# Performance work log

Hardware: AMD Instinct MI355X
Metric: run time of the kernel (lower is better)

## Reference

```python
import jax, jax.numpy as jnp
import numpy as np

N, K, D, GH = 19683, 26, 64, 32  # cells (27^3), max neighbors, state_size, gating hidden


def setup_inputs() -> dict:
    key = jax.random.key(0)
    ks = jax.random.split(key, 10)
    s = 0.1
    return {
        "current_state": jax.random.normal(ks[0], (N, D), jnp.float32),
        "neighbor_states": jax.random.normal(ks[1], (N, K, D), jnp.float32),
        "neighbor_cat": jax.random.randint(ks[2], (N, K), 0, 3),  # 0=local,1=functional,2=distant
        "W_local": s * jax.random.normal(ks[3], (2 * D, D), jnp.float32),
        "b_local": jnp.zeros((D,), jnp.float32),
        "W_f1": s * jax.random.normal(ks[4], (2 * D, 2 * D), jnp.float32),
        "b_f1": jnp.zeros((2 * D,), jnp.float32),
        "W_f2": s * jax.random.normal(ks[5], (2 * D, D), jnp.float32),
        "b_f2": jnp.zeros((D,), jnp.float32),
        "W_c1": s * jax.random.normal(ks[6], (2 * D, 2 * D), jnp.float32),
        "b_c1": jnp.zeros((2 * D,), jnp.float32),
        "W_c2": s * jax.random.normal(ks[7], (2 * D, D), jnp.float32),
        "b_c2": jnp.zeros((D,), jnp.float32),
        "W_g1": s * jax.random.normal(ks[8], (2 * D, GH), jnp.float32),
        "b_g1": jnp.zeros((GH,), jnp.float32),
        "W_g2": s * jax.random.normal(ks[9], (GH, 3), jnp.float32),
        "b_g2": jnp.zeros((3,), jnp.float32),
    }


def _masked_mean(nb, mask):
    # nb: [N,K,D], mask: [N,K] float -> mean over selected neighbors, count
    cnt = mask.sum(axis=1, keepdims=True)  # [N,1]
    mean = (nb * mask[..., None]).sum(axis=1) / jnp.maximum(cnt, 1.0)
    return mean, cnt


def reference(current_state, neighbor_states, neighbor_cat, W_local, b_local,
              W_f1, b_f1, W_f2, b_f2, W_c1, b_c1, W_c2, b_c2,
              W_g1, b_g1, W_g2, b_g2):
    cur, nb, cat = current_state, neighbor_states, neighbor_cat
    m_loc = (cat == 0).astype(cur.dtype)
    m_fun = (cat == 1).astype(cur.dtype)
    m_dst = (cat == 2).astype(cur.dtype)
    mean_l, cnt_l = _masked_mean(nb, m_loc)
    mean_f, cnt_f = _masked_mean(nb, m_fun)
    mean_d, cnt_d = _masked_mean(nb, m_dst)

    # local expert: SimpleLinear on [cur, local neighbor aggregate]
    out_l = jnp.tanh(jnp.concatenate([cur, mean_l], -1) @ W_local + b_local)
    out_l = jnp.where(cnt_l > 0, out_l, 0.0)  # zeros when no local neighbors

    # functional expert: HybridGNN-style 2-layer message MLP
    h = jnp.tanh(jnp.concatenate([cur, mean_f], -1) @ W_f1 + b_f1)
    out_f = jnp.tanh(h @ W_f2 + b_f2)
    out_f = jnp.where(cnt_f > 0, out_f, 0.0)

    # distant expert: lightweight CNF, 3 Euler integration steps
    x = cur
    dt = 1.0 / 3.0
    for _ in range(3):  # fixed integration_steps, not a data-dim loop
        v = jnp.tanh(jnp.concatenate([x, mean_d], -1) @ W_c1 + b_c1)
        x = x + dt * jnp.tanh(v @ W_c2 + b_c2)
    out_d = jnp.where(cnt_d > 0, x, 0.0)

    # gating network over [cur, neighbor_activity]
    act = nb.mean(axis=1)  # [N,D]
    g = jnp.tanh(jnp.concatenate([cur, act], -1) @ W_g1 + b_g1) @ W_g2 + b_g2
    w = jax.nn.softmax(g, axis=-1)  # [N,3]

    combined = w[:, 0:1] * out_l + w[:, 1:2] * out_f + w[:, 2:3] * out_d
    return combined, w
```

## Files before the change

kernel.cpp:

```cpp
#include <hip/hip_runtime.h>


#define NCELL 19683
#define KNB 26
#define NGROUP 1231
#define AGG_BLOCKS 2461
#define RP_BLOCKS 30
#define CUR_BLOCKS 616

typedef short bf16x8 __attribute__((ext_vector_type(8)));
typedef float f32x4 __attribute__((ext_vector_type(4)));

#define MEANB (NCELL * 64 * 2)
#define OFF_ML 0
#define OFF_MF (1 * MEANB)
#define OFF_MD (2 * MEANB)
#define OFF_ACT (3 * MEANB)
#define OFF_FLAGS (4 * MEANB)
#define OFF_RP (OFF_FLAGS + NCELL * 16)
#define OFF_CUR (OFF_RP + 120 * 1024)

#define FB_L 0
#define FB_F1 16
#define FB_F2 48
#define FB_C1 64
#define FB_C2 96
#define FB_G1 112

__device__ __forceinline__ unsigned short f2b(float f) {
  unsigned u; __builtin_memcpy(&u, &f, 4);
  u += 0x7FFFu + ((u >> 16) & 1u);
  return (unsigned short)(u >> 16);
}

__global__ __launch_bounds__(256) void k_prep(
    const float* __restrict__ nbp, const int* __restrict__ catp,
    const float* __restrict__ Wl, const float* __restrict__ Wf1,
    const float* __restrict__ Wf2, const float* __restrict__ Wc1,
    const float* __restrict__ Wc2, const float* __restrict__ Wg1,
    const float* __restrict__ curp, char* __restrict__ ws) {
  int bid = blockIdx.x;
  int tid = threadIdx.x;
  int lane = tid & 63;
  int wid = tid >> 6;

  if (bid < AGG_BLOCKS) {
    int half = lane >> 5;
    int l31 = lane & 31;
    int cell = bid * 8 + wid * 2 + half;
    int cc = min(cell, NCELL - 1);
    int myc = (l31 < KNB) ? catp[cc * KNB + l31] : -1;
    unsigned long long bl0 = __ballot(myc == 0);
    unsigned long long bl1 = __ballot(myc == 1);
    unsigned long long bl2 = __ballot(myc == 2);
    unsigned m0 = (unsigned)(bl0 >> (half * 32));
    unsigned m1 = (unsigned)(bl1 >> (half * 32));
    unsigned m2 = (unsigned)(bl2 >> (half * 32));
    float cl = (float)__popc(m0), cf = (float)__popc(m1), cd = (float)__popc(m2);

    const float* nbf = nbp + (size_t)cc * (KNB * 64) + l31 * 2;
    float sl0 = 0, sl1 = 0, sf0 = 0, sf1 = 0, sd0 = 0, sd1 = 0, sa0 = 0, sa1 = 0;
#pragma unroll
    for (int k = 0; k < KNB; k++) {
      float2 vf = *(const float2*)(nbf + k * 64);
      float v0 = vf.x, v1 = vf.y;
      int c = __shfl(myc, half * 32 + k);
      sa0 += v0; sa1 += v1;
      sl0 += (c == 0) ? v0 : 0.0f; sl1 += (c == 0) ? v1 : 0.0f;
      sf0 += (c == 1) ? v0 : 0.0f; sf1 += (c == 1) ? v1 : 0.0f;
      sd0 += (c == 2) ? v0 : 0.0f; sd1 += (c == 2) ? v1 : 0.0f;
    }
    float rl = 1.0f / fmaxf(cl, 1.0f);
    float rf = 1.0f / fmaxf(cf, 1.0f);
    float rd = 1.0f / fmaxf(cd, 1.0f);
    const float r26 = 1.0f / 26.0f;
    if (cell < NCELL) {
      int off = cell * 128 + l31 * 4;
      *(unsigned*)(ws + OFF_ML + off) = (unsigned)f2b(sl0 * rl) | ((unsigned)f2b(sl1 * rl) << 16);
      *(unsigned*)(ws + OFF_MF + off) = (unsigned)f2b(sf0 * rf) | ((unsigned)f2b(sf1 * rf) << 16);
      *(unsigned*)(ws + OFF_MD + off) = (unsigned)f2b(sd0 * rd) | ((unsigned)f2b(sd1 * rd) << 16);
      *(unsigned*)(ws + OFF_ACT + off) = (unsigned)f2b(sa0 * r26) | ((unsigned)f2b(sa1 * r26) << 16);
      if (l31 == 0) {
        float4 fl;
        fl.x = (cl > 0.0f) ? 1.0f : 0.0f;
        fl.y = (cf > 0.0f) ? 1.0f : 0.0f;
        fl.z = (cd > 0.0f) ? 1.0f : 0.0f;
        fl.w = 0.0f;
        *(float4*)(ws + OFF_FLAGS + cell * 16) = fl;
      }
    }
  } else if (bid < AGG_BLOCKS + RP_BLOCKS) {
    int frag = (bid - AGG_BLOCKS) * 4 + wid;
    if (frag >= 120) return;
    const float* src; int Nd, lf;
    if (frag < 16)       { src = Wl;  Nd = 64;  lf = frag; }
    else if (frag < 48)  { src = Wf1; Nd = 128; lf = frag - 16; }
    else if (frag < 64)  { src = Wf2; Nd = 64;  lf = frag - 48; }
    else if (frag < 96)  { src = Wc1; Nd = 128; lf = frag - 64; }
    else if (frag < 112) { src = Wc2; Nd = 64;  lf = frag - 96; }
    else                 { src = Wg1; Nd = 32;  lf = frag - 112; }
    int nt = lf >> 2, kt = lf & 3;
    int n = nt * 16 + (lane & 15);
    int k0 = kt * 32 + (lane >> 4) * 8;
    unsigned short o[8] __attribute__((aligned(16)));
#pragma unroll
    for (int j = 0; j < 8; j++) o[j] = f2b(src[(k0 + j) * Nd + n]);
    *(uint4*)(ws + OFF_RP + ((size_t)frag * 64 + lane) * 16) = *(const uint4*)o;
  } else {
    int idx = (bid - AGG_BLOCKS - RP_BLOCKS) * 256 + tid;
    if (idx >= NCELL * 8) return;
    float4 a = ((const float4*)curp)[idx * 2];
    float4 b = ((const float4*)curp)[idx * 2 + 1];
    uint4 o;
    o.x = (unsigned)f2b(a.x) | ((unsigned)f2b(a.y) << 16);
    o.y = (unsigned)f2b(a.z) | ((unsigned)f2b(a.w) << 16);
    o.z = (unsigned)f2b(b.x) | ((unsigned)f2b(b.y) << 16);
    o.w = (unsigned)f2b(b.z) | ((unsigned)f2b(b.w) << 16);
    ((uint4*)(ws + OFF_CUR))[idx] = o;
  }
}

__device__ __forceinline__ void stage64(const uint4* __restrict__ src, int g, uint4* dst, int lane) {
#pragma unroll
  for (int i = 0; i < 2; i++) {
    int idx = min(g * 128 + i * 64 + lane, NCELL * 8 - 1);
    uint4 v = src[idx];
    int local = i * 64 + lane;
    int cell = local >> 3, c = local & 7;
    dst[cell * 8 + (c ^ (cell & 7))] = v;
  }
}
__device__ __forceinline__ void afrags2(const uint4* lo, const uint4* hi, int m, int q, bf16x8* a) {
#pragma unroll
  for (int kt = 0; kt < 4; kt++) {
    const uint4* b = (kt < 2) ? lo : hi;
    int ch = ((kt & 1) * 4 + q) ^ (m & 7);
    a[kt] = *(const bf16x8*)&b[m * 8 + ch];
  }
}
__device__ __forceinline__ void afragsS(const uint4* sb, int m, int q, bf16x8* a) {
#pragma unroll
  for (int kt = 0; kt < 4; kt++) {
    int ch = (kt * 4 + q) ^ m;
    a[kt] = *(const bf16x8*)&sb[m * 16 + ch];
  }
}
template <int NT>
__device__ __forceinline__ void gemmN(const bf16x8* __restrict__ wf, int fb, const bf16x8* a,
                                      int lane, f32x4* out) {
#pragma unroll
  for (int nt = 0; nt < NT; nt++) {
    f32x4 acc = {0.f, 0.f, 0.f, 0.f};
#pragma unroll
    for (int kt = 0; kt < 4; kt++) {
      bf16x8 b = wf[(fb + nt * 4 + kt) * 64 + lane];
      acc = __builtin_amdgcn_mfma_f32_16x16x32_bf16(a[kt], b, acc, 0, 0, 0);
    }
    out[nt] = acc;
  }
}
__device__ __forceinline__ void store_sb(uint4* sb, int cell, int feat, float v) {
  ((unsigned short*)&sb[cell * 16 + ((feat >> 3) ^ cell)])[feat & 7] = f2b(v);
}
__device__ __forceinline__ void store_xb(uint4* xb, int cell, int feat, float v) {
  ((unsigned short*)&xb[cell * 8 + ((feat >> 3) ^ (cell & 7))])[feat & 7] = f2b(v);
}

__global__ __launch_bounds__(256) void k_mlp(
    const float* __restrict__ curp,
    const float* __restrict__ bl_, const float* __restrict__ bf1_,
    const float* __restrict__ bf2_, const float* __restrict__ bc1_,
    const float* __restrict__ bc2_, const float* __restrict__ bg1_,
    const float* __restrict__ Wg2, const float* __restrict__ bg2_,
    const char* __restrict__ ws, float* __restrict__ outp) {
  __shared__ uint4 smem[4 * 640];
  int tid = threadIdx.x, lane = tid & 63, wv = tid >> 6;
  int g = blockIdx.x * 4 + wv;
  if (g >= NGROUP) return;
  uint4* wbase = smem + wv * 640;
  uint4* curb = wbase;
  uint4* mb = wbase + 128;
  uint4* xb = wbase + 256;
  uint4* sb = wbase + 384;

  const unsigned short* curh = (const unsigned short*)(ws + OFF_CUR);
  int m = lane & 15, q = lane >> 4;
  const bf16x8* wf = (const bf16x8*)(ws + OFF_RP);
  bf16x8 a[4];

  stage64((const uint4*)curh, g, curb, lane);
  stage64((const uint4*)(ws + OFF_ML), g, mb, lane);
  afrags2(curb, mb, m, q, a);
  f32x4 ol[4];
  gemmN<4>(wf, FB_L, a, lane, ol);
#pragma unroll
  for (int nt = 0; nt < 4; nt++) {
    float bb = bl_[nt * 16 + m];
#pragma unroll
    for (int r = 0; r < 4; r++) ol[nt][r] = tanhf(ol[nt][r] + bb);
  }

  stage64((const uint4*)(ws + OFF_MF), g, mb, lane);
  afrags2(curb, mb, m, q, a);
  f32x4 h8[8];
  gemmN<8>(wf, FB_F1, a, lane, h8);
#pragma unroll
  for (int nt = 0; nt < 8; nt++) {
    float bb = bf1_[nt * 16 + m];
#pragma unroll
    for (int r = 0; r < 4; r++) store_sb(sb, q * 4 + r, nt * 16 + m, tanhf(h8[nt][r] + bb));
  }
  afragsS(sb, m, q, a);
  f32x4 of[4];
  gemmN<4>(wf, FB_F2, a, lane, of);
#pragma unroll
  for (int nt = 0; nt < 4; nt++) {
    float bb = bf2_[nt * 16 + m];
#pragma unroll
    for (int r = 0; r < 4; r++) of[nt][r] = tanhf(of[nt][r] + bb);
  }

  stage64((const uint4*)(ws + OFF_ACT), g, mb, lane);
  afrags2(curb, mb, m, q, a);
  f32x4 gh[2];
  gemmN<2>(wf, FB_G1, a, lane, gh);
#pragma unroll
  for (int nt = 0; nt < 2; nt++) {
    float bb = bg1_[nt * 16 + m];
#pragma unroll
    for (int r = 0; r < 4; r++) gh[nt][r] = tanhf(gh[nt][r] + bb);
  }
  float w2v[2][3];
#pragma unroll
  for (int nt = 0; nt < 2; nt++)
#pragma unroll
    for (int t = 0; t < 3; t++) w2v[nt][t] = Wg2[(nt * 16 + m) * 3 + t];
  float bg2v[3];
#pragma unroll
  for (int t = 0; t < 3; t++) bg2v[t] = bg2_[t];
  float w0[4], w1[4], w2[4];
#pragma unroll
  for (int r = 0; r < 4; r++) {
    float gv[3];
#pragma unroll
    for (int t = 0; t < 3; t++) {
      float p = gh[0][r] * w2v[0][t] + gh[1][r] * w2v[1][t];
      p += __shfl_xor(p, 1); p += __shfl_xor(p, 2); p += __shfl_xor(p, 4); p += __shfl_xor(p, 8);
      gv[t] = p + bg2v[t];
    }
    float mx = fmaxf(gv[0], fmaxf(gv[1], gv[2]));
    float e0 = expf(gv[0] - mx), e1 = expf(gv[1] - mx), e2 = expf(gv[2] - mx);
    float rs = 1.0f / (e0 + e1 + e2);
    w0[r] = e0 * rs; w1[r] = e1 * rs; w2[r] = e2 * rs;
    int cell = g * 16 + q * 4 + r;
    if (cell < NCELL && m < 3) {
      float wsel = (m == 0) ? w0[r] : (m == 1) ? w1[r] : w2[r];
      outp[(size_t)NCELL * 64 + cell * 3 + m] = wsel;
    }
  }

  stage64((const uint4*)(ws + OFF_MD), g, mb, lane);
  float xr[4][4];
#pragma unroll
  for (int nt = 0; nt < 4; nt++)
#pragma unroll
    for (int r = 0; r < 4; r++) {
      int cell = min(g * 16 + q * 4 + r, NCELL - 1);
      xr[nt][r] = curp[(size_t)cell * 64 + nt * 16 + m];
    }
  for (int step = 0; step < 3; step++) {
#pragma unroll
    for (int nt = 0; nt < 4; nt++)
#pragma unroll
      for (int r = 0; r < 4; r++) store_xb(xb, q * 4 + r, nt * 16 + m, xr[nt][r]);
    afrags2(xb, mb, m, q, a);
    f32x4 v8[8];
    gemmN<8>(wf, FB_C1, a, lane, v8);
#pragma unroll
    for (int nt = 0; nt < 8; nt++) {
      float bb = bc1_[nt * 16 + m];
#pragma unroll
      for (int r = 0; r < 4; r++) store_sb(sb, q * 4 + r, nt * 16 + m, tanhf(v8[nt][r] + bb));
    }
    afragsS(sb, m, q, a);
    f32x4 dx[4];
    gemmN<4>(wf, FB_C2, a, lane, dx);
#pragma unroll
    for (int nt = 0; nt < 4; nt++) {
      float bb = bc2_[nt * 16 + m];
#pragma unroll
      for (int r = 0; r < 4; r++) xr[nt][r] += (1.0f / 3.0f) * tanhf(dx[nt][r] + bb);
    }
  }

  float4 flg[4];
  const float4* flp = (const float4*)(ws + OFF_FLAGS);
#pragma unroll
  for (int r = 0; r < 4; r++) flg[r] = flp[min(g * 16 + q * 4 + r, NCELL - 1)];
#pragma unroll
  for (int nt = 0; nt < 4; nt++)
#pragma unroll
    for (int r = 0; r < 4; r++) {
      float res = w0[r] * flg[r].x * ol[nt][r] + w1[r] * flg[r].y * of[nt][r] +
                  w2[r] * flg[r].z * xr[nt][r];
      int cell = g * 16 + q * 4 + r;
      if (cell < NCELL) outp[(size_t)cell * 64 + nt * 16 + m] = res;
    }
}

extern "C" void kernel_launch(void* const* d_in, const int* in_sizes, int n_in,
                              void* d_out, int out_size, void* d_ws, size_t ws_size,
                              hipStream_t stream) {
  const float* cur = (const float*)d_in[0];
  const float* nb  = (const float*)d_in[1];
  const int* cat   = (const int*)d_in[2];
  const float* Wl  = (const float*)d_in[3];
  const float* bl  = (const float*)d_in[4];
  const float* Wf1 = (const float*)d_in[5];
  const float* bf1 = (const float*)d_in[6];
  const float* Wf2 = (const float*)d_in[7];
  const float* bf2 = (const float*)d_in[8];
  const float* Wc1 = (const float*)d_in[9];
  const float* bc1 = (const float*)d_in[10];
  const float* Wc2 = (const float*)d_in[11];
  const float* bc2 = (const float*)d_in[12];
  const float* Wg1 = (const float*)d_in[13];
  const float* bg1 = (const float*)d_in[14];
  const float* Wg2 = (const float*)d_in[15];
  const float* bg2 = (const float*)d_in[16];
  char* ws = (char*)d_ws;
  float* outp = (float*)d_out;

  k_prep<<<AGG_BLOCKS + RP_BLOCKS + CUR_BLOCKS, 256, 0, stream>>>(
      nb, cat, Wl, Wf1, Wf2, Wc1, Wc2, Wg1, cur, ws);
  k_mlp<<<(NGROUP + 3) / 4, 256, 0, stream>>>(cur, bl, bf1, bf2, bc1, bc2, bg1, Wg2, bg2,
                                              (const char*)ws, outp);
}
```

Baseline: 303.1 us.

## Fuse neighbor aggregation into MLP kernel and split experts across waves

Neighbor aggregation now runs inside the main kernel, and the means go straight into shared memory, so the bf16 mean buffers no longer make a round trip through global memory. Each 256-thread block handles 16 cells, with work split by wave: wave 0 runs the local expert and gating, wave 1 the functional expert, and waves 2-3 share the CNF steps, synchronising through barriers. tanhf/expf are replaced by fast exp/rcp approximations. The cost is extra block barriers, idle waves 0-1 during the CNF steps, and slightly lower accuracy in tanh.

```diff
diff --git a/kernel.cpp b/kernel.cpp
--- a/kernel.cpp
+++ b/kernel.cpp
@@ -3,22 +3,10 @@
 
 #define NCELL 19683
 #define KNB 26
-#define NGROUP 1231
-#define AGG_BLOCKS 2461
-#define RP_BLOCKS 30
-#define CUR_BLOCKS 616
+#define NGRP 1231
 
 typedef short bf16x8 __attribute__((ext_vector_type(8)));
 typedef float f32x4 __attribute__((ext_vector_type(4)));
-
-#define MEANB (NCELL * 64 * 2)
-#define OFF_ML 0
-#define OFF_MF (1 * MEANB)
-#define OFF_MD (2 * MEANB)
-#define OFF_ACT (3 * MEANB)
-#define OFF_FLAGS (4 * MEANB)
-#define OFF_RP (OFF_FLAGS + NCELL * 16)
-#define OFF_CUR (OFF_RP + 120 * 1024)
 
 #define FB_L 0
 #define FB_F1 16
@@ -32,280 +20,299 @@
   u += 0x7FFFu + ((u >> 16) & 1u);
   return (unsigned short)(u >> 16);
 }
-
-__global__ __launch_bounds__(256) void k_prep(
-    const float* __restrict__ nbp, const int* __restrict__ catp,
+__device__ __forceinline__ unsigned pack2(float x, float y) {
+  return (unsigned)f2b(x) | ((unsigned)f2b(y) << 16);
+}
+__device__ __forceinline__ float tanh_fast(float x) {
+  float e = __expf(2.0f * x);
+  return 1.0f - 2.0f * __builtin_amdgcn_rcpf(e + 1.0f);
+}
+
+__global__ __launch_bounds__(256) void k_repack(
     const float* __restrict__ Wl, const float* __restrict__ Wf1,
     const float* __restrict__ Wf2, const float* __restrict__ Wc1,
     const float* __restrict__ Wc2, const float* __restrict__ Wg1,
-    const float* __restrict__ curp, char* __restrict__ ws) {
-  int bid = blockIdx.x;
-  int tid = threadIdx.x;
-  int lane = tid & 63;
-  int wid = tid >> 6;
-
-  if (bid < AGG_BLOCKS) {
-    int half = lane >> 5;
-    int l31 = lane & 31;
-    int cell = bid * 8 + wid * 2 + half;
-    int cc = min(cell, NCELL - 1);
-    int myc = (l31 < KNB) ? catp[cc * KNB + l31] : -1;
-    unsigned long long bl0 = __ballot(myc == 0);
-    unsigned long long bl1 = __ballot(myc == 1);
-    unsigned long long bl2 = __ballot(myc == 2);
-    unsigned m0 = (unsigned)(bl0 >> (half * 32));
-    unsigned m1 = (unsigned)(bl1 >> (half * 32));
-    unsigned m2 = (unsigned)(bl2 >> (half * 32));
+    char* __restrict__ ws) {
+  int frag = blockIdx.x * 4 + (threadIdx.x >> 6);
+  int lane = threadIdx.x & 63;
+  if (frag >= 120) return;
+  const float* src; int Nd, lf;
+  if (frag < 16)       { src = Wl;  Nd = 64;  lf = frag; }
+  else if (frag < 48)  { src = Wf1; Nd = 128; lf = frag - 16; }
+  else if (frag < 64)  { src = Wf2; Nd = 64;  lf = frag - 48; }
+  else if (frag < 96)  { src = Wc1; Nd = 128; lf = frag - 64; }
+  else if (frag < 112) { src = Wc2; Nd = 64;  lf = frag - 96; }
+  else                 { src = Wg1; Nd = 32;  lf = frag - 112; }
+  int nt = lf >> 2, kt = lf & 3;
+  int n = nt * 16 + (lane & 15);
+  int k0 = kt * 32 + (lane >> 4) * 8;
+  unsigned short o[8] __attribute__((aligned(16)));
+#pragma unroll
+  for (int j = 0; j < 8; j++) o[j] = f2b(src[(k0 + j) * Nd + n]);
+  *(uint4*)(ws + ((size_t)frag * 64 + lane) * 16) = *(const uint4*)o;
+}
+
+__device__ __forceinline__ void afrags2(const uint4* lo, const uint4* hi, int m, int q, bf16x8* a) {
+#pragma unroll
+  for (int kt = 0; kt < 4; kt++) {
+    const uint4* b = (kt < 2) ? lo : hi;
+    int ch = ((kt & 1) * 4 + q) ^ (m & 7);
+    a[kt] = *(const bf16x8*)&b[m * 8 + ch];
+  }
+}
+__device__ __forceinline__ void afragsS(const uint4* sb, int m, int q, bf16x8* a) {
+#pragma unroll
+  for (int kt = 0; kt < 4; kt++) {
+    int ch = (kt * 4 + q) ^ m;
+    a[kt] = *(const bf16x8*)&sb[m * 16 + ch];
+  }
+}
+template <int NT>
+__device__ __forceinline__ void gemmN(const bf16x8* __restrict__ wf, int fb, const bf16x8* a,
+                                      int lane, f32x4* out) {
+#pragma unroll
+  for (int nt = 0; nt < NT; nt++) {
+    f32x4 acc = {0.f, 0.f, 0.f, 0.f};
+#pragma unroll
+    for (int kt = 0; kt < 4; kt++) {
+      bf16x8 b = wf[(fb + nt * 4 + kt) * 64 + lane];
+      acc = __builtin_amdgcn_mfma_f32_16x16x32_bf16(a[kt], b, acc, 0, 0, 0);
+    }
+    out[nt] = acc;
+  }
+}
+__device__ __forceinline__ void store_sb(uint4* sb, int cell, int feat, float v) {
+  ((unsigned short*)&sb[cell * 16 + ((feat >> 3) ^ cell)])[feat & 7] = f2b(v);
+}
+__device__ __forceinline__ void store_xb(uint4* xb, int cell, int feat, float v) {
+  ((unsigned short*)&xb[cell * 8 + ((feat >> 3) ^ (cell & 7))])[feat & 7] = f2b(v);
+}
+
+__global__ __launch_bounds__(256, 4) void k_main(
+    const float* __restrict__ curp, const float* __restrict__ nbp, const int* __restrict__ catp,
+    const float* __restrict__ bl_, const float* __restrict__ bf1_, const float* __restrict__ bf2_,
+    const float* __restrict__ bc1_, const float* __restrict__ bc2_, const float* __restrict__ bg1_,
+    const float* __restrict__ Wg2, const float* __restrict__ bg2_,
+    const char* __restrict__ ws, float* __restrict__ outp) {
+  __shared__ uint4 smem[2080];
+  uint4* curb = smem;
+  uint4* mlb  = smem + 128;
+  uint4* mfb  = smem + 256;
+  uint4* mdb  = smem + 384;
+  uint4* actb = smem + 512;
+  uint4* xb   = smem + 640;
+  uint4* sbF  = smem + 768;
+  uint4* sbC  = smem + 1024;
+  float* outL = (float*)(smem + 1280);
+  float* outF = (float*)(smem + 1536);
+  float* outD = (float*)(smem + 1792);
+  float4* flagsb = (float4*)(smem + 2048);
+  float4* wvalsb = (float4*)(smem + 2064);
+
+  int tid = threadIdx.x, lane = tid & 63, wv = tid >> 6;
+  int g = blockIdx.x;
+
+  {
+    int cq = lane >> 4, fq = lane & 15;
+    int cellLoc = wv * 4 + cq;
+    int cell = min(g * 16 + cellLoc, NCELL - 1);
+    int c0 = catp[cell * KNB + fq];
+    int c1 = (fq < KNB - 16) ? catp[cell * KNB + 16 + fq] : -1;
+    unsigned long long B0a = __ballot(c0 == 0), B1a = __ballot(c0 == 1), B2a = __ballot(c0 == 2);
+    unsigned long long B0b = __ballot(c1 == 0), B1b = __ballot(c1 == 1), B2b = __ballot(c1 == 2);
+    int sh = cq * 16;
+    unsigned m0 = (unsigned)((B0a >> sh) & 0xFFFFull) | ((unsigned)((B0b >> sh) & 0x3FFull) << 16);
+    unsigned m1 = (unsigned)((B1a >> sh) & 0xFFFFull) | ((unsigned)((B1b >> sh) & 0x3FFull) << 16);
+    unsigned m2 = (unsigned)((B2a >> sh) & 0xFFFFull) | ((unsigned)((B2b >> sh) & 0x3FFull) << 16);
     float cl = (float)__popc(m0), cf = (float)__popc(m1), cd = (float)__popc(m2);
-
-    const float* nbf = nbp + (size_t)cc * (KNB * 64) + l31 * 2;
-    float sl0 = 0, sl1 = 0, sf0 = 0, sf1 = 0, sd0 = 0, sd1 = 0, sa0 = 0, sa1 = 0;
+    float sl[4] = {0, 0, 0, 0}, sf[4] = {0, 0, 0, 0}, sd[4] = {0, 0, 0, 0}, sa[4] = {0, 0, 0, 0};
+    const float* nbc = nbp + (size_t)cell * (KNB * 64) + fq * 4;
 #pragma unroll
     for (int k = 0; k < KNB; k++) {
-      float2 vf = *(const float2*)(nbf + k * 64);
-      float v0 = vf.x, v1 = vf.y;
-      int c = __shfl(myc, half * 32 + k);
-      sa0 += v0; sa1 += v1;
-      sl0 += (c == 0) ? v0 : 0.0f; sl1 += (c == 0) ? v1 : 0.0f;
-      sf0 += (c == 1) ? v0 : 0.0f; sf1 += (c == 1) ? v1 : 0.0f;
-      sd0 += (c == 2) ? v0 : 0.0f; sd1 += (c == 2) ? v1 : 0.0f;
+      float4 v = *(const float4*)(nbc + k * 64);
+      float b0 = (float)((m0 >> k) & 1u);
+      float b1 = (float)((m1 >> k) & 1u);
+      float b2 = (float)((m2 >> k) & 1u);
+      sa[0] += v.x; sa[1] += v.y; sa[2] += v.z; sa[3] += v.w;
+      sl[0] += b0 * v.x; sl[1] += b0 * v.y; sl[2] += b0 * v.z; sl[3] += b0 * v.w;
+      sf[0] += b1 * v.x; sf[1] += b1 * v.y; sf[2] += b1 * v.z; sf[3] += b1 * v.w;
+      sd[0] += b2 * v.x; sd[1] += b2 * v.y; sd[2] += b2 * v.z; sd[3] += b2 * v.w;
     }
     float rl = 1.0f / fmaxf(cl, 1.0f);
     float rf = 1.0f / fmaxf(cf, 1.0f);
     float rd = 1.0f / fmaxf(cd, 1.0f);
     const float r26 = 1.0f / 26.0f;
+    int ch = (fq >> 1) ^ (cellLoc & 7);
+    int sub = fq & 1;
+    ((uint2*)&mlb[cellLoc * 8 + ch])[sub] =
+        make_uint2(pack2(sl[0] * rl, sl[1] * rl), pack2(sl[2] * rl, sl[3] * rl));
+    ((uint2*)&mfb[cellLoc * 8 + ch])[sub] =
+        make_uint2(pack2(sf[0] * rf, sf[1] * rf), pack2(sf[2] * rf, sf[3] * rf));
+    ((uint2*)&mdb[cellLoc * 8 + ch])[sub] =
+        make_uint2(pack2(sd[0] * rd, sd[1] * rd), pack2(sd[2] * rd, sd[3] * rd));
+    ((uint2*)&actb[cellLoc * 8 + ch])[sub] =
+        make_uint2(pack2(sa[0] * r26, sa[1] * r26), pack2(sa[2] * r26, sa[3] * r26));
+    if (fq == 0)
+      flagsb[cellLoc] = make_float4(cl > 0.f ? 1.f : 0.f, cf > 0.f ? 1.f : 0.f,
+                                    cd > 0.f ? 1.f : 0.f, 0.f);
+  }
+  if (tid < 128) {
+    int cellLoc = tid >> 3, c = tid & 7;
+    int cell = min(g * 16 + cellLoc, NCELL - 1);
+    const float4* cp = (const float4*)(curp + (size_t)cell * 64) + c * 2;
+    float4 A = cp[0], B = cp[1];
+    uint4 o;
+    o.x = pack2(A.x, A.y); o.y = pack2(A.z, A.w);
+    o.z = pack2(B.x, B.y); o.w = pack2(B.z, B.w);
+    curb[cellLoc * 8 + (c ^ (cellLoc & 7))] = o;
+  }
+
+  int m = lane & 15, q = lane >> 4;
+  const bf16x8* wf = (const bf16x8*)ws;
+  bf16x8 a4[4];
+  float xr[2][4];
+
+  if (wv >= 2) {
+    int ntb = (wv - 2) * 2;
+#pragma unroll
+    for (int j = 0; j < 2; j++)
+#pragma unroll
+      for (int r = 0; r < 4; r++) {
+        int cell = min(g * 16 + q * 4 + r, NCELL - 1);
+        xr[j][r] = curp[(size_t)cell * 64 + (ntb + j) * 16 + m];
+      }
+  }
+  __syncthreads();
+
+  if (wv == 0) {
+    afrags2(curb, mlb, m, q, a4);
+    f32x4 ol[4];
+    gemmN<4>(wf, FB_L, a4, lane, ol);
+#pragma unroll
+    for (int nt = 0; nt < 4; nt++) {
+      float bb = bl_[nt * 16 + m];
+#pragma unroll
+      for (int r = 0; r < 4; r++) outL[(q * 4 + r) * 64 + nt * 16 + m] = tanh_fast(ol[nt][r] + bb);
+    }
+    afrags2(curb, actb, m, q, a4);
+    f32x4 gh[2];
+    gemmN<2>(wf, FB_G1, a4, lane, gh);
+#pragma unroll
+    for (int nt = 0; nt < 2; nt++) {
+      float bb = bg1_[nt * 16 + m];
+#pragma unroll
+      for (int r = 0; r < 4; r++) gh[nt][r] = tanh_fast(gh[nt][r] + bb);
+    }
+    float w2v[2][3];
+#pragma unroll
+    for (int nt = 0; nt < 2; nt++)
+#pragma unroll
+      for (int t = 0; t < 3; t++) w2v[nt][t] = Wg2[(nt * 16 + m) * 3 + t];
+    float bg2v[3] = {bg2_[0], bg2_[1], bg2_[2]};
+#pragma unroll
+    for (int r = 0; r < 4; r++) {
+      float gv[3];
+#pragma unroll
+      for (int t = 0; t < 3; t++) {
+        float p = gh[0][r] * w2v[0][t] + gh[1][r] * w2v[1][t];
+        p += __shfl_xor(p, 1); p += __shfl_xor(p, 2); p += __shfl_xor(p, 4); p += __shfl_xor(p, 8);
+        gv[t] = p + bg2v[t];
+      }
+      float mx = fmaxf(gv[0], fmaxf(gv[1], gv[2]));
+      float e0 = __expf(gv[0] - mx), e1 = __expf(gv[1] - mx), e2 = __expf(gv[2] - mx);
+      float rs = __builtin_amdgcn_rcpf(e0 + e1 + e2);
+      int cellLoc = q * 4 + r;
+      int cell = g * 16 + cellLoc;
+      if (m == 0) wvalsb[cellLoc] = make_float4(e0 * rs, e1 * rs, e2 * rs, 0.f);
+      if (cell < NCELL && m < 3) {
+        float wsel = (m == 0) ? e0 * rs : (m == 1) ? e1 * rs : e2 * rs;
+        outp[(size_t)NCELL * 64 + cell * 3 + m] = wsel;
+      }
+    }
+  } else if (wv == 1) {
+    afrags2(curb, mfb, m, q, a4);
+    f32x4 h8[8];
+    gemmN<8>(wf, FB_F1, a4, lane, h8);
+#pragma unroll
+    for (int nt = 0; nt < 8; nt++) {
+      float bb = bf1_[nt * 16 + m];
+#pragma unroll
+      for (int r = 0; r < 4; r++)
+        store_sb(sbF, q * 4 + r, nt * 16 + m, tanh_fast(h8[nt][r] + bb));
+    }
+    afragsS(sbF, m, q, a4);
+    f32x4 of4[4];
+    gemmN<4>(wf, FB_F2, a4, lane, of4);
+#pragma unroll
+    for (int nt = 0; nt < 4; nt++) {
+      float bb = bf2_[nt * 16 + m];
+#pragma unroll
+      for (int r = 0; r < 4; r++)
+        outF[(q * 4 + r) * 64 + nt * 16 + m] = tanh_fast(of4[nt][r] + bb);
+    }
+  } else {
+    int ntb = (wv - 2) * 2;
+#pragma unroll
+    for (int j = 0; j < 2; j++)
+#pragma unroll
+      for (int r = 0; r < 4; r++) store_xb(xb, q * 4 + r, (ntb + j) * 16 + m, xr[j][r]);
+  }
+
+  for (int step = 0; step < 3; step++) {
+    __syncthreads();
+    if (wv >= 2) {
+      int hb = (wv - 2) * 4;
+      afrags2(xb, mdb, m, q, a4);
+      f32x4 v4[4];
+      gemmN<4>(wf, FB_C1 + hb * 4, a4, lane, v4);
+#pragma unroll
+      for (int j = 0; j < 4; j++) {
+        int nt = hb + j;
+        float bb = bc1_[nt * 16 + m];
+#pragma unroll
+        for (int r = 0; r < 4; r++)
+          store_sb(sbC, q * 4 + r, nt * 16 + m, tanh_fast(v4[j][r] + bb));
+      }
+    }
+    __syncthreads();
+    if (wv >= 2) {
+      int ntb = (wv - 2) * 2;
+      afragsS(sbC, m, q, a4);
+      f32x4 dx2[2];
+      gemmN<2>(wf, FB_C2 + ntb * 4, a4, lane, dx2);
+#pragma unroll
+      for (int j = 0; j < 2; j++) {
+        int nt = ntb + j;
+        float bb = bc2_[nt * 16 + m];
+#pragma unroll
+        for (int r = 0; r < 4; r++) {
+          xr[j][r] += (1.0f / 3.0f) * tanh_fast(dx2[j][r] + bb);
+          if (step < 2) store_xb(xb, q * 4 + r, nt * 16 + m, xr[j][r]);
+          else outD[(q * 4 + r) * 64 + nt * 16 + m] = xr[j][r];
+        }
+      }
+    }
+  }
+  __syncthreads();
+
+  {
+    int cellLoc = tid >> 4, fi = tid & 15;
+    float4 vl = ((const float4*)outL)[cellLoc * 16 + fi];
+    float4 vf = ((const float4*)outF)[cellLoc * 16 + fi];
+    float4 vd = ((const float4*)outD)[cellLoc * 16 + fi];
+    float4 fl = flagsb[cellLoc];
+    float4 wv4 = wvalsb[cellLoc];
+    float a0 = wv4.x * fl.x, a1 = wv4.y * fl.y, a2 = wv4.z * fl.z;
+    int cell = g * 16 + cellLoc;
     if (cell < NCELL) {
-      int off = cell * 128 + l31 * 4;
-      *(unsigned*)(ws + OFF_ML + off) = (unsigned)f2b(sl0 * rl) | ((unsigned)f2b(sl1 * rl) << 16);
-      *(unsigned*)(ws + OFF_MF + off) = (unsigned)f2b(sf0 * rf) | ((unsigned)f2b(sf1 * rf) << 16);
-      *(unsigned*)(ws + OFF_MD + off) = (unsigned)f2b(sd0 * rd) | ((unsigned)f2b(sd1 * rd) << 16);
-      *(unsigned*)(ws + OFF_ACT + off) = (unsigned)f2b(sa0 * r26) | ((unsigned)f2b(sa1 * r26) << 16);
-      if (l31 == 0) {
-        float4 fl;
-        fl.x = (cl > 0.0f) ? 1.0f : 0.0f;
-        fl.y = (cf > 0.0f) ? 1.0f : 0.0f;
-        fl.z = (cd > 0.0f) ? 1.0f : 0.0f;
-        fl.w = 0.0f;
-        *(float4*)(ws + OFF_FLAGS + cell * 16) = fl;
-      }
-    }
-  } else if (bid < AGG_BLOCKS + RP_BLOCKS) {
-    int frag = (bid - AGG_BLOCKS) * 4 + wid;
-    if (frag >= 120) return;
-    const float* src; int Nd, lf;
-    if (frag < 16)       { src = Wl;  Nd = 64;  lf = frag; }
-    else if (frag < 48)  { src = Wf1; Nd = 128; lf = frag - 16; }
-    else if (frag < 64)  { src = Wf2; Nd = 64;  lf = frag - 48; }
-    else if (frag < 96)  { src = Wc1; Nd = 128; lf = frag - 64; }
-    else if (frag < 112) { src = Wc2; Nd = 64;  lf = frag - 96; }
-    else                 { src = Wg1; Nd = 32;  lf = frag - 112; }
-    int nt = lf >> 2, kt = lf & 3;
-    int n = nt * 16 + (lane & 15);
-    int k0 = kt * 32 + (lane >> 4) * 8;
-    unsigned short o[8] __attribute__((aligned(16)));
-#pragma unroll
-    for (int j = 0; j < 8; j++) o[j] = f2b(src[(k0 + j) * Nd + n]);
-    *(uint4*)(ws + OFF_RP + ((size_t)frag * 64 + lane) * 16) = *(const uint4*)o;
-  } else {
-    int idx = (bid - AGG_BLOCKS - RP_BLOCKS) * 256 + tid;
-    if (idx >= NCELL * 8) return;
-    float4 a = ((const float4*)curp)[idx * 2];
-    float4 b = ((const float4*)curp)[idx * 2 + 1];
-    uint4 o;
-    o.x = (unsigned)f2b(a.x) | ((unsigned)f2b(a.y) << 16);
-    o.y = (unsigned)f2b(a.z) | ((unsigned)f2b(a.w) << 16);
-    o.z = (unsigned)f2b(b.x) | ((unsigned)f2b(b.y) << 16);
-    o.w = (unsigned)f2b(b.z) | ((unsigned)f2b(b.w) << 16);
-    ((uint4*)(ws + OFF_CUR))[idx] = o;
-  }
-}
-
-__device__ __forceinline__ void stage64(const uint4* __restrict__ src, int g, uint4* dst, int lane) {
-#pragma unroll
-  for (int i = 0; i < 2; i++) {
-    int idx = min(g * 128 + i * 64 + lane, NCELL * 8 - 1);
-    uint4 v = src[idx];
-    int local = i * 64 + lane;
-    int cell = local >> 3, c = local & 7;
-    dst[cell * 8 + (c ^ (cell & 7))] = v;
-  }
-}
-__device__ __forceinline__ void afrags2(const uint4* lo, const uint4* hi, int m, int q, bf16x8* a) {
-#pragma unroll
-  for (int kt = 0; kt < 4; kt++) {
-    const uint4* b = (kt < 2) ? lo : hi;
-    int ch = ((kt & 1) * 4 + q) ^ (m & 7);
-    a[kt] = *(const bf16x8*)&b[m * 8 + ch];
-  }
-}
-__device__ __forceinline__ void afragsS(const uint4* sb, int m, int q, bf16x8* a) {
-#pragma unroll
-  for (int kt = 0; kt < 4; kt++) {
-    int ch = (kt * 4 + q) ^ m;
-    a[kt] = *(const bf16x8*)&sb[m * 16 + ch];
-  }
-}
-template <int NT>
-__device__ __forceinline__ void gemmN(const bf16x8* __restrict__ wf, int fb, const bf16x8* a,
-                                      int lane, f32x4* out) {
-#pragma unroll
-  for (int nt = 0; nt < NT; nt++) {
-    f32x4 acc = {0.f, 0.f, 0.f, 0.f};
-#pragma unroll
-    for (int kt = 0; kt < 4; kt++) {
-      bf16x8 b = wf[(fb + nt * 4 + kt) * 64 + lane];
-      acc = __builtin_amdgcn_mfma_f32_16x16x32_bf16(a[kt], b, acc, 0, 0, 0);
-    }
-    out[nt] = acc;
-  }
-}
-__device__ __forceinline__ void store_sb(uint4* sb, int cell, int feat, float v) {
-  ((unsigned short*)&sb[cell * 16 + ((feat >> 3) ^ cell)])[feat & 7] = f2b(v);
-}
-__device__ __forceinline__ void store_xb(uint4* xb, int cell, int feat, float v) {
-  ((unsigned short*)&xb[cell * 8 + ((feat >> 3) ^ (cell & 7))])[feat & 7] = f2b(v);
-}
-
-__global__ __launch_bounds__(256) void k_mlp(
-    const float* __restrict__ curp,
-    const float* __restrict__ bl_, const float* __restrict__ bf1_,
-    const float* __restrict__ bf2_, const float* __restrict__ bc1_,
-    const float* __restrict__ bc2_, const float* __restrict__ bg1_,
-    const float* __restrict__ Wg2, const float* __restrict__ bg2_,
-    const char* __restrict__ ws, float* __restrict__ outp) {
-  __shared__ uint4 smem[4 * 640];
-  int tid = threadIdx.x, lane = tid & 63, wv = tid >> 6;
-  int g = blockIdx.x * 4 + wv;
-  if (g >= NGROUP) return;
-  uint4* wbase = smem + wv * 640;
-  uint4* curb = wbase;
-  uint4* mb = wbase + 128;
-  uint4* xb = wbase + 256;
-  uint4* sb = wbase + 384;
-
-  const unsigned short* curh = (const unsigned short*)(ws + OFF_CUR);
-  int m = lane & 15, q = lane >> 4;
-  const bf16x8* wf = (const bf16x8*)(ws + OFF_RP);
-  bf16x8 a[4];
-
-  stage64((const uint4*)curh, g, curb, lane);
-  stage64((const uint4*)(ws + OFF_ML), g, mb, lane);
-  afrags2(curb, mb, m, q, a);
-  f32x4 ol[4];
-  gemmN<4>(wf, FB_L, a, lane, ol);
-#pragma unroll
-  for (int nt = 0; nt < 4; nt++) {
-    float bb = bl_[nt * 16 + m];
-#pragma unroll
-    for (int r = 0; r < 4; r++) ol[nt][r] = tanhf(ol[nt][r] + bb);
-  }
-
-  stage64((const uint4*)(ws + OFF_MF), g, mb, lane);
-  afrags2(curb, mb, m, q, a);
-  f32x4 h8[8];
-  gemmN<8>(wf, FB_F1, a, lane, h8);
-#pragma unroll
-  for (int nt = 0; nt < 8; nt++) {
-    float bb = bf1_[nt * 16 + m];
-#pragma unroll
-    for (int r = 0; r < 4; r++) store_sb(sb, q * 4 + r, nt * 16 + m, tanhf(h8[nt][r] + bb));
-  }
-  afragsS(sb, m, q, a);
-  f32x4 of[4];
-  gemmN<4>(wf, FB_F2, a, lane, of);
-#pragma unroll
-  for (int nt = 0; nt < 4; nt++) {
-    float bb = bf2_[nt * 16 + m];
-#pragma unroll
-    for (int r = 0; r < 4; r++) of[nt][r] = tanhf(of[nt][r] + bb);
-  }
-
-  stage64((const uint4*)(ws + OFF_ACT), g, mb, lane);
-  afrags2(curb, mb, m, q, a);
-  f32x4 gh[2];
-  gemmN<2>(wf, FB_G1, a, lane, gh);
-#pragma unroll
-  for (int nt = 0; nt < 2; nt++) {
-    float bb = bg1_[nt * 16 + m];
-#pragma unroll
-    for (int r = 0; r < 4; r++) gh[nt][r] = tanhf(gh[nt][r] + bb);
-  }
-  float w2v[2][3];
-#pragma unroll
-  for (int nt = 0; nt < 2; nt++)
-#pragma unroll
-    for (int t = 0; t < 3; t++) w2v[nt][t] = Wg2[(nt * 16 + m) * 3 + t];
-  float bg2v[3];
-#pragma unroll
-  for (int t = 0; t < 3; t++) bg2v[t] = bg2_[t];
-  float w0[4], w1[4], w2[4];
-#pragma unroll
-  for (int r = 0; r < 4; r++) {
-    float gv[3];
-#pragma unroll
-    for (int t = 0; t < 3; t++) {
-      float p = gh[0][r] * w2v[0][t] + gh[1][r] * w2v[1][t];
-      p += __shfl_xor(p, 1); p += __shfl_xor(p, 2); p += __shfl_xor(p, 4); p += __shfl_xor(p, 8);
-      gv[t] = p + bg2v[t];
-    }
-    float mx = fmaxf(gv[0], fmaxf(gv[1], gv[2]));
-    float e0 = expf(gv[0] - mx), e1 = expf(gv[1] - mx), e2 = expf(gv[2] - mx);
-    float rs = 1.0f / (e0 + e1 + e2);
-    w0[r] = e0 * rs; w1[r] = e1 * rs; w2[r] = e2 * rs;
-    int cell = g * 16 + q * 4 + r;
-    if (cell < NCELL && m < 3) {
-      float wsel = (m == 0) ? w0[r] : (m == 1) ? w1[r] : w2[r];
-      outp[(size_t)NCELL * 64 + cell * 3 + m] = wsel;
-    }
-  }
-
-  stage64((const uint4*)(ws + OFF_MD), g, mb, lane);
-  float xr[4][4];
-#pragma unroll
-  for (int nt = 0; nt < 4; nt++)
-#pragma unroll
-    for (int r = 0; r < 4; r++) {
-      int cell = min(g * 16 + q * 4 + r, NCELL - 1);
-      xr[nt][r] = curp[(size_t)cell * 64 + nt * 16 + m];
-    }
-  for (int step = 0; step < 3; step++) {
-#pragma unroll
-    for (int nt = 0; nt < 4; nt++)
-#pragma unroll
-      for (int r = 0; r < 4; r++) store_xb(xb, q * 4 + r, nt * 16 + m, xr[nt][r]);
-    afrags2(xb, mb, m, q, a);
-    f32x4 v8[8];
-    gemmN<8>(wf, FB_C1, a, lane, v8);
-#pragma unroll
-    for (int nt = 0; nt < 8; nt++) {
-      float bb = bc1_[nt * 16 + m];
-#pragma unroll
-      for (int r = 0; r < 4; r++) store_sb(sb, q * 4 + r, nt * 16 + m, tanhf(v8[nt][r] + bb));
-    }
-    afragsS(sb, m, q, a);
-    f32x4 dx[4];
-    gemmN<4>(wf, FB_C2, a, lane, dx);
-#pragma unroll
-    for (int nt = 0; nt < 4; nt++) {
-      float bb = bc2_[nt * 16 + m];
-#pragma unroll
-      for (int r = 0; r < 4; r++) xr[nt][r] += (1.0f / 3.0f) * tanhf(dx[nt][r] + bb);
-    }
-  }
-
-  float4 flg[4];
-  const float4* flp = (const float4*)(ws + OFF_FLAGS);
-#pragma unroll
-  for (int r = 0; r < 4; r++) flg[r] = flp[min(g * 16 + q * 4 + r, NCELL - 1)];
-#pragma unroll
-  for (int nt = 0; nt < 4; nt++)
-#pragma unroll
-    for (int r = 0; r < 4; r++) {
-      float res = w0[r] * flg[r].x * ol[nt][r] + w1[r] * flg[r].y * of[nt][r] +
-                  w2[r] * flg[r].z * xr[nt][r];
-      int cell = g * 16 + q * 4 + r;
-      if (cell < NCELL) outp[(size_t)cell * 64 + nt * 16 + m] = res;
-    }
+      float4 res;
+      res.x = a0 * vl.x + a1 * vf.x + a2 * vd.x;
+      res.y = a0 * vl.y + a1 * vf.y + a2 * vd.y;
+      res.z = a0 * vl.z + a1 * vf.z + a2 * vd.z;
+      res.w = a0 * vl.w + a1 * vf.w + a2 * vd.w;
+      ((float4*)(outp + (size_t)cell * 64))[fi] = res;
+    }
+  }
 }
 
 extern "C" void kernel_launch(void* const* d_in, const int* in_sizes, int n_in,
@@ -331,8 +338,7 @@
   char* ws = (char*)d_ws;
   float* outp = (float*)d_out;
 
-  k_prep<<<AGG_BLOCKS + RP_BLOCKS + CUR_BLOCKS, 256, 0, stream>>>(
-      nb, cat, Wl, Wf1, Wf2, Wc1, Wc2, Wg1, cur, ws);
-  k_mlp<<<(NGROUP + 3) / 4, 256, 0, stream>>>(cur, bl, bf1, bf2, bc1, bc2, bg1, Wg2, bg2,
-                                              (const char*)ws, outp);
-}
+  k_repack<<<30, 256, 0, stream>>>(Wl, Wf1, Wf2, Wc1, Wc2, Wg1, ws);
+  k_main<<<NGRP, 256, 0, stream>>>(cur, nb, cat, bl, bf1, bf2, bc1, bc2, bg1, Wg2, bg2,
+                                   (const char*)ws, outp);
+}
```

Measured after the change: 248.7 us. -17.9%, faster.
